# Optimization experiments

Hardware: AMD Instinct MI355X
Metric: run time of the kernel (lower is better)

Reference implementation:

```python
import jax, jax.numpy as jnp
import numpy as np

N = 50000      # nodes
E = 400000     # edges
F = 64         # feature_size
H = 4          # heads
D = 16         # embedding_size (per-head dim)
HD = H * D     # concat hidden = 64
ED = 16        # edge_dim
L = 3          # model_layers (extra TransformerConv layers)
DN = 256       # dense_neurons
G = 128        # number of graphs in the batch
SCALE = float(1.0 / np.sqrt(D))


def setup_inputs() -> dict:
    key = jax.random.key(0)
    ks = jax.random.split(key, 40)

    def w(k, shape, fan_in):
        return jax.random.normal(k, shape, jnp.float32) / np.float32(np.sqrt(fan_in))

    inp = {}
    inp["x"] = jax.random.normal(ks[0], (N, F), jnp.float32)
    inp["edge_attr"] = jax.random.normal(ks[1], (E, ED), jnp.float32)
    inp["edge_index"] = jax.random.randint(ks[2], (2, E), 0, N)
    inp["batch"] = jnp.sort(jax.random.randint(ks[3], (N,), 0, G))

    # conv1: feature_size -> heads*embedding
    inp["Wq0"] = w(ks[4], (F, HD), F); inp["bq0"] = jnp.zeros((HD,), jnp.float32)
    inp["Wk0"] = w(ks[5], (F, HD), F); inp["bk0"] = jnp.zeros((HD,), jnp.float32)
    inp["Wv0"] = w(ks[6], (F, HD), F); inp["bv0"] = jnp.zeros((HD,), jnp.float32)
    inp["We0"] = w(ks[7], (ED, HD), ED)                      # lin_edge, no bias
    inp["Ws0"] = w(ks[8], (F, HD), F); inp["bs0"] = jnp.zeros((HD,), jnp.float32)  # lin_skip
    inp["Wb0"] = w(ks[9], (3 * HD, 1), 3 * HD)               # lin_beta, no bias

    # stacked layers 1..L: heads*embedding -> heads*embedding
    inp["Wq"] = w(ks[10], (L, HD, HD), HD); inp["bq"] = jnp.zeros((L, HD), jnp.float32)
    inp["Wk"] = w(ks[11], (L, HD, HD), HD); inp["bk"] = jnp.zeros((L, HD), jnp.float32)
    inp["Wv"] = w(ks[12], (L, HD, HD), HD); inp["bv"] = jnp.zeros((L, HD), jnp.float32)
    inp["We"] = w(ks[13], (L, ED, HD), ED)
    inp["Ws"] = w(ks[14], (L, HD, HD), HD); inp["bs"] = jnp.zeros((L, HD), jnp.float32)
    inp["Wb"] = w(ks[15], (L, 3 * HD, 1), 3 * HD)

    # MLP head: Linear(2*HD -> DN), Linear(DN -> 1)
    inp["Wlin"] = w(ks[16], (2 * HD, DN), 2 * HD); inp["blin"] = jnp.zeros((DN,), jnp.float32)
    inp["Wout"] = w(ks[17], (DN, 1), DN); inp["bout"] = jnp.zeros((1,), jnp.float32)
    return inp


def _tconv(x, edge_attr, src, dst, Wq, bq, Wk, bk, Wv, bv, We, Ws, bs, Wb):
    """PyG TransformerConv (concat=True, beta=True, edge_dim), eval mode (no dropout)."""
    n = x.shape[0]
    q = (x @ Wq + bq).reshape(n, H, D)
    k = (x @ Wk + bk).reshape(n, H, D)
    v = (x @ Wv + bv).reshape(n, H, D)
    e = (edge_attr @ We).reshape(-1, H, D)
    ke = k[src] + e                                   # [E,H,D] keys with edge feats
    ve = v[src] + e                                   # [E,H,D] values with edge feats
    logits = jnp.einsum('ehd,ehd->eh', q[dst], ke) * SCALE
    # segment softmax over incoming edges of each target node
    m = jax.ops.segment_max(logits, dst, num_segments=n)
    p = jnp.exp(logits - m[dst])
    s = jax.ops.segment_sum(p, dst, num_segments=n)
    a = p / (s[dst] + 1e-16)                          # [E,H]
    agg = jax.ops.segment_sum(a[:, :, None] * ve, dst, num_segments=n).reshape(n, HD)
    skip = x @ Ws + bs                                # root/skip transform
    beta = jax.nn.sigmoid(jnp.concatenate([agg, skip, agg - skip], axis=-1) @ Wb)
    return beta * skip + (1.0 - beta) * agg


def reference(x, edge_attr, edge_index, batch,
              Wq0, bq0, Wk0, bk0, Wv0, bv0, We0, Ws0, bs0, Wb0,
              Wq, bq, Wk, bk, Wv, bv, We, Ws, bs, Wb,
              Wlin, blin, Wout, bout):
    src, dst = edge_index[0], edge_index[1]
    h = jax.nn.relu(_tconv(x, edge_attr, src, dst,
                           Wq0, bq0, Wk0, bk0, Wv0, bv0, We0, Ws0, bs0, Wb0))
    for i in range(L):
        h = jax.nn.relu(_tconv(h, edge_attr, src, dst,
                               Wq[i], bq[i], Wk[i], bk[i], Wv[i], bv[i],
                               We[i], Ws[i], bs[i], Wb[i]))
    # global max pool (gmp) and global mean pool (gap)
    cnt = jax.ops.segment_sum(jnp.ones((h.shape[0],), h.dtype), batch, num_segments=G)
    gmax = jax.ops.segment_max(h, batch, num_segments=G)
    gmax = jnp.where(cnt[:, None] > 0, gmax, 0.0)
    gmean = jax.ops.segment_sum(h, batch, num_segments=G) / jnp.maximum(cnt[:, None], 1.0)
    z = jnp.concatenate([gmax, gmean], axis=-1) @ Wlin + blin
    return jax.nn.sigmoid(z @ Wout + bout)
```

## Files before the change

### kernel.cpp

```cpp
#include <hip/hip_runtime.h>
#include <math.h>

#define SCALEF 0.25f

typedef __attribute__((ext_vector_type(8))) short short8;
typedef __attribute__((ext_vector_type(4))) float f32x4;

__device__ __forceinline__ unsigned short f2bf(float x) {
  unsigned u = __float_as_uint(x);
  unsigned r = u + 0x7FFFu + ((u >> 16) & 1u);
  return (unsigned short)(r >> 16);
}
__device__ __forceinline__ float bf2f(unsigned short h) {
  return __uint_as_float(((unsigned)h) << 16);
}

__global__ void k_hist(const int* __restrict__ dst, int* __restrict__ counts, int E) {
  int i = blockIdx.x * 256 + threadIdx.x;
  if (i < E) atomicAdd(&counts[dst[i]], 1);
}

__global__ __launch_bounds__(1024) void k_scan1(const int* __restrict__ counts,
                                                int* __restrict__ excl,
                                                int* __restrict__ bsums, int n) {
  __shared__ int sd[1024];
  int t = threadIdx.x;
  int i = blockIdx.x * 1024 + t;
  int v = (i < n) ? counts[i] : 0;
  sd[t] = v;
  __syncthreads();
  for (int off = 1; off < 1024; off <<= 1) {
    int x = (t >= off) ? sd[t - off] : 0;
    __syncthreads();
    sd[t] += x;
    __syncthreads();
  }
  if (i < n) excl[i] = sd[t] - v;
  if (t == 1023) bsums[blockIdx.x] = sd[1023];
}

__global__ void k_scan2(int* bsums, int nb) {
  if (threadIdx.x == 0 && blockIdx.x == 0) {
    int run = 0;
    for (int i = 0; i < nb; ++i) { int v = bsums[i]; bsums[i] = run; run += v; }
  }
}

__global__ __launch_bounds__(1024) void k_scan3(int* __restrict__ rowptr, int* __restrict__ cursor,
                                                const int* __restrict__ bsums, int n, int Etot) {
  int i = blockIdx.x * 1024 + threadIdx.x;
  if (i < n) { int v = rowptr[i] + bsums[blockIdx.x]; rowptr[i] = v; cursor[i] = v; }
  if (i == 0) rowptr[n] = Etot;
}

__global__ void k_scatter(const int* __restrict__ dst, int* __restrict__ cursor,
                          int* __restrict__ colidx, int E) {
  int i = blockIdx.x * 256 + threadIdx.x;
  if (i < E) { int pos = atomicAdd(&cursor[dst[i]], 1); colidx[pos] = i; }
}

__global__ void k_perm(const int* __restrict__ colidx, const int* __restrict__ esrc,
                       const float* __restrict__ EA, int* __restrict__ esrcp,
                       unsigned short* __restrict__ EAp, int E) {
  int r = blockIdx.x * 256 + threadIdx.x;
  if (r >= E) return;
  const int eid = colidx[r];
  esrcp[r] = esrc[eid] * 128;
  const float4* s4 = (const float4*)(EA + ((size_t)eid << 4));
  float4 a = s4[0], b = s4[1], c = s4[2], d = s4[3];
  union { unsigned short us[16]; uint4 u4[2]; } o;
  o.us[0] = f2bf(a.x); o.us[1] = f2bf(a.y); o.us[2] = f2bf(a.z); o.us[3] = f2bf(a.w);
  o.us[4] = f2bf(b.x); o.us[5] = f2bf(b.y); o.us[6] = f2bf(b.z); o.us[7] = f2bf(b.w);
  o.us[8] = f2bf(c.x); o.us[9] = f2bf(c.y); o.us[10] = f2bf(c.z); o.us[11] = f2bf(c.w);
  o.us[12] = f2bf(d.x); o.us[13] = f2bf(d.y); o.us[14] = f2bf(d.z); o.us[15] = f2bf(d.w);
  uint4* d4 = (uint4*)(EAp + ((size_t)r << 4));
  d4[0] = o.u4[0]; d4[1] = o.u4[1];
}

__global__ __launch_bounds__(256) void k_wqt(
    const float* __restrict__ Wq0, const float* __restrict__ bq0, const float* __restrict__ We0,
    const float* __restrict__ Wq, const float* __restrict__ bq, const float* __restrict__ We,
    float* __restrict__ Wqt, float* __restrict__ bqt) {
  const int l = blockIdx.x;
  const float* wq = (l == 0) ? Wq0 : Wq + (l - 1) * 4096;
  const float* bv = (l == 0) ? bq0 : bq + (l - 1) * 64;
  const float* we = (l == 0) ? We0 : We + (l - 1) * 1024;
  float* out  = Wqt + l * 4096;
  float* outb = bqt + l * 64;
  const int t = threadIdx.x;
  const int r = t >> 2;
  const int hh = t & 3;
  float wqr[16];
  #pragma unroll
  for (int d = 0; d < 16; ++d) wqr[d] = wq[r * 64 + hh * 16 + d];
  #pragma unroll
  for (int bb = 0; bb < 16; ++bb) {
    float s = 0.f;
    #pragma unroll
    for (int d = 0; d < 16; ++d) s += wqr[d] * we[bb * 64 + hh * 16 + d];
    out[r * 64 + hh * 16 + bb] = s * SCALEF;
  }
  if (r == 0) {
    #pragma unroll
    for (int bb = 0; bb < 16; ++bb) {
      float s = 0.f;
      #pragma unroll
      for (int d = 0; d < 16; ++d) s += bv[hh * 16 + d] * we[bb * 64 + hh * 16 + d];
      outb[hh * 16 + bb] = s * SCALEF;
    }
  }
}

__global__ void k_wprep(
    const float* __restrict__ Wq0, const float* __restrict__ Wk0, const float* __restrict__ Wv0,
    const float* __restrict__ Ws0,
    const float* __restrict__ Wq, const float* __restrict__ Wk, const float* __restrict__ Wv,
    const float* __restrict__ Ws, const float* __restrict__ Wqt,
    const float* __restrict__ bq0, const float* __restrict__ bk0, const float* __restrict__ bv0,
    const float* __restrict__ bs0,
    const float* __restrict__ bq, const float* __restrict__ bk, const float* __restrict__ bv,
    const float* __restrict__ bs, const float* __restrict__ bqt,
    unsigned short* __restrict__ WT, float* __restrict__ bcat) {
  const int id = blockIdx.x * 256 + threadIdx.x;
  if (id >= 4 * 5 * 4096) return;
  const int l = id / 20480;
  const int rem = id - l * 20480;
  const int mat = rem >> 12;
  const int idx = rem & 4095;
  const int k = idx >> 6;
  const int c = idx & 63;
  float v;
  if (mat == 0)      v = (l == 0) ? Wq0[idx] : Wq[(l - 1) * 4096 + idx];
  else if (mat == 1) v = (l == 0) ? Wk0[idx] : Wk[(l - 1) * 4096 + idx];
  else if (mat == 2) v = (l == 0) ? Wv0[idx] : Wv[(l - 1) * 4096 + idx];
  else if (mat == 3) v = (l == 0) ? Ws0[idx] : Ws[(l - 1) * 4096 + idx];
  else               v = Wqt[l * 4096 + idx];
  WT[(size_t)(l * 5 + mat) * 4096 + c * 64 + k] = f2bf(v);
  if (k == 0) {
    float b;
    if (mat == 0)      b = (l == 0) ? bq0[c] : bq[(l - 1) * 64 + c];
    else if (mat == 1) b = (l == 0) ? bk0[c] : bk[(l - 1) * 64 + c];
    else if (mat == 2) b = (l == 0) ? bv0[c] : bv[(l - 1) * 64 + c];
    else if (mat == 3) b = (l == 0) ? bs0[c] : bs[(l - 1) * 64 + c];
    else               b = bqt[l * 64 + c];
    bcat[(l * 5 + mat) * 64 + c] = b;
  }
}

__global__ void k_xcast(const float* __restrict__ x, unsigned short* __restrict__ xb, int n4) {
  int i = blockIdx.x * 256 + threadIdx.x;
  if (i < n4) {
    float4 v = ((const float4*)x)[i];
    ushort4 o;
    o.x = f2bf(v.x); o.y = f2bf(v.y); o.z = f2bf(v.z); o.w = f2bf(v.w);
    ((ushort4*)xb)[i] = o;
  }
}

__global__ __launch_bounds__(256) void k_linm(
    const unsigned short* __restrict__ Xb, const unsigned short* __restrict__ WT,
    const float* __restrict__ bcat,
    unsigned short* __restrict__ Qb, unsigned short* __restrict__ Kb,
    unsigned short* __restrict__ Vb, unsigned short* __restrict__ Sb,
    unsigned short* __restrict__ Tb, int n) {
  const int lane = threadIdx.x & 63;
  const int tile = blockIdx.x * 4 + (threadIdx.x >> 6);
  const int ntr = n >> 4;
  if (tile >= ntr) return;
  const int r0 = tile << 4;
  const int c15 = lane & 15;
  const int kg = lane >> 4;
  const int rbase = r0 + kg * 4;

  const unsigned short* xrow = Xb + (size_t)(r0 + c15) * 64 + kg * 8;
  const short8 a0 = *(const short8*)(xrow);
  const short8 a1 = *(const short8*)(xrow + 32);

  #pragma unroll
  for (int mat = 0; mat < 5; ++mat) {
    const unsigned short* wb = WT + ((size_t)mat << 12) + (size_t)c15 * 64 + kg * 8;
    f32x4 acc0 = {0.f, 0.f, 0.f, 0.f}, acc1 = acc0, acc2 = acc0, acc3 = acc0;
    {
      short8 b0 = *(const short8*)(wb);
      short8 b1 = *(const short8*)(wb + 32);
      acc0 = __builtin_amdgcn_mfma_f32_16x16x32_bf16(a0, b0, acc0, 0, 0, 0);
      acc0 = __builtin_amdgcn_mfma_f32_16x16x32_bf16(a1, b1, acc0, 0, 0, 0);
    }
    {
      short8 b0 = *(const short8*)(wb + 16 * 64);
      short8 b1 = *(const short8*)(wb + 16 * 64 + 32);
      acc1 = __builtin_amdgcn_mfma_f32_16x16x32_bf16(a0, b0, acc1, 0, 0, 0);
      acc1 = __builtin_amdgcn_mfma_f32_16x16x32_bf16(a1, b1, acc1, 0, 0, 0);
    }
    {
      short8 b0 = *(const short8*)(wb + 32 * 64);
      short8 b1 = *(const short8*)(wb + 32 * 64 + 32);
      acc2 = __builtin_amdgcn_mfma_f32_16x16x32_bf16(a0, b0, acc2, 0, 0, 0);
      acc2 = __builtin_amdgcn_mfma_f32_16x16x32_bf16(a1, b1, acc2, 0, 0, 0);
    }
    {
      short8 b0 = *(const short8*)(wb + 48 * 64);
      short8 b1 = *(const short8*)(wb + 48 * 64 + 32);
      acc3 = __builtin_amdgcn_mfma_f32_16x16x32_bf16(a0, b0, acc3, 0, 0, 0);
      acc3 = __builtin_amdgcn_mfma_f32_16x16x32_bf16(a1, b1, acc3, 0, 0, 0);
    }

    const float* bb = bcat + mat * 64;
    const float bi0 = bb[c15], bi1 = bb[16 + c15], bi2 = bb[32 + c15], bi3 = bb[48 + c15];

    unsigned short* O = (mat == 0) ? Qb : (mat == 1) ? Kb : (mat == 2) ? Vb
                      : (mat == 3) ? Sb : Tb;
    #pragma unroll
    for (int reg = 0; reg < 4; ++reg) {
      const size_t ro = (size_t)(rbase + reg) * 64;
      O[ro + c15]      = f2bf(acc0[reg] + bi0);
      O[ro + 16 + c15] = f2bf(acc1[reg] + bi1);
      O[ro + 32 + c15] = f2bf(acc2[reg] + bi2);
      O[ro + 48 + c15] = f2bf(acc3[reg] + bi3);
    }
  }
}

#define LOADST(KK, VV, EE, jj) do {                                       \
    int jc_ = (jj) < mc ? (jj) : mc - 1;                                  \
    int off_ = __builtin_amdgcn_readlane(snv, jc_);                       \
    KK = *(const unsigned short*)(kbase + off_);                          \
    VV = *(const unsigned short*)(vbase + off_);                          \
    EE = eabase[(size_t)(c0 + jc_) << 4];                                 \
  } while (0)

#define COMPUTE(KK, VV, EE, jj) do {                                      \
    if ((jj) < mc) {                                                      \
      const float ef = bf2f(EE);                                          \
      float pl = qv * bf2f(KK) + tl * ef;                                 \
      pl += __shfl_xor(pl, 1, 64);                                        \
      pl += __shfl_xor(pl, 2, 64);                                        \
      pl += __shfl_xor(pl, 4, 64);                                        \
      pl += __shfl_xor(pl, 8, 64);                                        \
      const float p = __expf(pl);                                         \
      ssum += p;                                                          \
      accv += p * bf2f(VV);                                               \
      accw += p * ef;                                                     \
    }                                                                     \
  } while (0)

__global__ __launch_bounds__(128, 6) void k_attn(
    const unsigned short* __restrict__ Qb, const unsigned short* __restrict__ Kb,
    const unsigned short* __restrict__ Vb, const unsigned short* __restrict__ Tb,
    const unsigned short* __restrict__ Sb, const unsigned short* __restrict__ EAp,
    const int* __restrict__ esrcp, const int* __restrict__ rowptr,
    const float* __restrict__ We, const float* __restrict__ Wb,
    unsigned short* __restrict__ Hout, int n) {
  const int t = threadIdx.x;
  const int lane = t & 63;
  const int node = blockIdx.x * 2 + (t >> 6);
  if (node >= n) return;

  const float qv = bf2f(Qb[(size_t)node * 64 + lane]) * SCALEF;
  const float tl = bf2f(Tb[(size_t)node * 64 + lane]);
  const int r0 = rowptr[node], r1 = rowptr[node + 1];

  const char* kbase = (const char*)Kb + 2 * lane;
  const char* vbase = (const char*)Vb + 2 * lane;
  const unsigned short* eabase = EAp + (lane & 15);

  float ssum = 0.f, accv = 0.f, accw = 0.f;

  for (int c0 = r0; c0 < r1; c0 += 64) {
    const int mc = min(64, r1 - c0);
    int snv = 0;
    if (lane < mc) snv = esrcp[c0 + lane];

    unsigned short kA, vA, kB, vB, kC, vC, kD, vD;
    unsigned short eA, eB, eC, eD;
    LOADST(kA, vA, eA, 0);
    LOADST(kB, vB, eB, 1);
    LOADST(kC, vC, eC, 2);
    LOADST(kD, vD, eD, 3);

    for (int j = 0; j < mc; j += 4) {
      COMPUTE(kA, vA, eA, j);     LOADST(kA, vA, eA, j + 4);
      COMPUTE(kB, vB, eB, j + 1); LOADST(kB, vB, eB, j + 5);
      COMPUTE(kC, vC, eC, j + 2); LOADST(kC, vC, eC, j + 6);
      COMPUTE(kD, vD, eD, j + 3); LOADST(kD, vD, eD, j + 7);
    }
  }

  float agg = accv;
  #pragma unroll
  for (int j = 0; j < 16; ++j) {
    const float wj = __shfl(accw, (lane & 48) | j, 64);
    agg += wj * We[j * 64 + lane];
  }
  agg /= (ssum + 1e-16f);

  const float sk = bf2f(Sb[(size_t)node * 64 + lane]);
  float contrib = agg * Wb[lane] + sk * Wb[64 + lane] + (agg - sk) * Wb[128 + lane];
  #pragma unroll
  for (int off = 1; off < 64; off <<= 1) contrib += __shfl_xor(contrib, off, 64);
  const float beta = 1.f / (1.f + __expf(-contrib));
  const float o = beta * sk + (1.f - beta) * agg;
  Hout[(size_t)node * 64 + lane] = f2bf(fmaxf(o, 0.f));
}

__global__ __launch_bounds__(256) void k_pool(const unsigned short* __restrict__ Hf,
    const int* __restrict__ batch,
    float* __restrict__ gmax, float* __restrict__ gmean, int n) {
  const int g = blockIdx.x;
  const int lane = threadIdx.x & 63;
  const int w = threadIdx.x >> 6;

  int a = 0, b = n;
  while (a < b) { int mid = (a + b) >> 1; if (batch[mid] < g) a = mid + 1; else b = mid; }
  const int lo = a;
  b = n;
  while (a < b) { int mid = (a + b) >> 1; if (batch[mid] < g + 1) a = mid + 1; else b = mid; }
  const int hi = a;

  float vmax = -1e30f, vsum = 0.f;
  for (int i = lo + w; i < hi; i += 4) {
    const float v = bf2f(Hf[(size_t)i * 64 + lane]);
    vmax = fmaxf(vmax, v);
    vsum += v;
  }
  __shared__ float smax[4][64], ssum[4][64];
  smax[w][lane] = vmax;
  ssum[w][lane] = vsum;
  __syncthreads();
  if (w == 0) {
    const float mx = fmaxf(fmaxf(smax[0][lane], smax[1][lane]),
                           fmaxf(smax[2][lane], smax[3][lane]));
    const float sm = ssum[0][lane] + ssum[1][lane] + ssum[2][lane] + ssum[3][lane];
    const int cnt = hi - lo;
    gmax[g * 64 + lane]  = (cnt > 0) ? mx : 0.f;
    gmean[g * 64 + lane] = sm / fmaxf((float)cnt, 1.f);
  }
}

__global__ __launch_bounds__(256) void k_mlp(const float* __restrict__ gmax,
    const float* __restrict__ gmean,
    const float* __restrict__ Wlin, const float* __restrict__ blin,
    const float* __restrict__ Wout, const float* __restrict__ bout,
    float* __restrict__ out, int G) {
  __shared__ float cat[128];
  __shared__ float red[4];
  const int g = blockIdx.x;
  const int t = threadIdx.x;
  if (t < 64) cat[t] = gmax[g * 64 + t];
  else if (t < 128) cat[t] = gmean[g * 64 + (t - 64)];
  __syncthreads();
  float acc = blin[t];
  for (int j = 0; j < 128; ++j) acc += cat[j] * Wlin[j * 256 + t];
  float p = acc * Wout[t];
  #pragma unroll
  for (int off = 1; off < 64; off <<= 1) p += __shfl_xor(p, off, 64);
  if ((t & 63) == 0) red[t >> 6] = p;
  __syncthreads();
  if (t == 0) {
    const float z = red[0] + red[1] + red[2] + red[3] + bout[0];
    out[g] = 1.f / (1.f + __expf(-z));
  }
}

extern "C" void kernel_launch(void* const* d_in, const int* in_sizes, int n_in,
                              void* d_out, int out_size, void* d_ws, size_t ws_size,
                              hipStream_t stream) {
  const float* x     = (const float*)d_in[0];
  const float* ea    = (const float*)d_in[1];
  const int*   eidx  = (const int*)d_in[2];
  const int*   batch = (const int*)d_in[3];
  const float *Wq0 = (const float*)d_in[4],  *bq0 = (const float*)d_in[5];
  const float *Wk0 = (const float*)d_in[6],  *bk0 = (const float*)d_in[7];
  const float *Wv0 = (const float*)d_in[8],  *bv0 = (const float*)d_in[9];
  const float *We0 = (const float*)d_in[10];
  const float *Ws0 = (const float*)d_in[11], *bs0 = (const float*)d_in[12];
  const float *Wb0 = (const float*)d_in[13];
  const float *Wq  = (const float*)d_in[14], *bq  = (const float*)d_in[15];
  const float *Wk  = (const float*)d_in[16], *bk  = (const float*)d_in[17];
  const float *Wv  = (const float*)d_in[18], *bv  = (const float*)d_in[19];
  const float *We  = (const float*)d_in[20];
  const float *Ws  = (const float*)d_in[21], *bs  = (const float*)d_in[22];
  const float *Wb  = (const float*)d_in[23];
  const float *Wlin = (const float*)d_in[24], *blin = (const float*)d_in[25];
  const float *Wout = (const float*)d_in[26], *bout = (const float*)d_in[27];

  const int N = in_sizes[0] / 64;
  const int E = in_sizes[2] / 2;
  const int G = out_size;
  const int* esrc = eidx;
  const int* edst = eidx + E;

  char* wsp = (char*)d_ws;
  auto alloc = [&](size_t bytes) -> void* {
    void* p = (void*)wsp;
    wsp += (bytes + 255) & ~(size_t)255;
    return p;
  };
  unsigned short* Qb = (unsigned short*)alloc((size_t)N * 64 * 2);
  unsigned short* Kb = (unsigned short*)alloc((size_t)N * 64 * 2);
  unsigned short* Vb = (unsigned short*)alloc((size_t)N * 64 * 2);
  unsigned short* Tb = (unsigned short*)alloc((size_t)N * 64 * 2);
  unsigned short* Sb16 = (unsigned short*)alloc((size_t)N * 64 * 2);
  unsigned short* Hb16 = (unsigned short*)alloc((size_t)N * 64 * 2);
  unsigned short* Xb16 = (unsigned short*)alloc((size_t)N * 64 * 2);
  int* counts  = (int*)alloc((size_t)N * 4);
  int* rowptr  = (int*)alloc((size_t)(N + 1) * 4);
  int* cursor  = (int*)alloc((size_t)N * 4);
  int* colidx  = (int*)alloc((size_t)E * 4);
  int* bsums   = (int*)alloc(1024 * 4);
  int* esrcp   = (int*)alloc((size_t)E * 4);
  unsigned short* EAp = (unsigned short*)alloc((size_t)E * 16 * 2);
  float* Wqt   = (float*)alloc(4 * 4096 * 4);
  float* bqt   = (float*)alloc(4 * 64 * 4);
  unsigned short* WT = (unsigned short*)alloc(4 * 5 * 4096 * 2);
  float* bcat  = (float*)alloc(4 * 5 * 64 * 4);
  float* gmaxf  = (float*)alloc((size_t)G * 64 * 4);
  float* gmeanf = (float*)alloc((size_t)G * 64 * 4);

  const int gridE = (E + 255) / 256;
  const int NB1 = (N + 1023) / 1024;
  hipMemsetAsync(counts, 0, (size_t)N * 4, stream);
  k_hist<<<gridE, 256, 0, stream>>>(edst, counts, E);
  k_scan1<<<NB1, 1024, 0, stream>>>(counts, rowptr, bsums, N);
  k_scan2<<<1, 64, 0, stream>>>(bsums, NB1);
  k_scan3<<<NB1, 1024, 0, stream>>>(rowptr, cursor, bsums, N, E);
  k_scatter<<<gridE, 256, 0, stream>>>(edst, cursor, colidx, E);
  k_perm<<<gridE, 256, 0, stream>>>(colidx, esrc, ea, esrcp, EAp, E);
  k_wqt<<<4, 256, 0, stream>>>(Wq0, bq0, We0, Wq, bq, We, Wqt, bqt);
  k_wprep<<<(4 * 5 * 4096 + 255) / 256, 256, 0, stream>>>(
      Wq0, Wk0, Wv0, Ws0, Wq, Wk, Wv, Ws, Wqt,
      bq0, bk0, bv0, bs0, bq, bk, bv, bs, bqt, WT, bcat);
  k_xcast<<<(N * 16 + 255) / 256, 256, 0, stream>>>(x, Xb16, N * 16);

  const int gridLinM = ((N >> 4) + 3) / 4;
  const int gridAttn = (N + 1) / 2;
  for (int l = 0; l < 4; ++l) {
    const float* we_ = (l == 0) ? We0 : We + (l - 1) * 1024;
    const float* wb_ = (l == 0) ? Wb0 : Wb + (l - 1) * 192;
    const unsigned short* xin = (l == 0) ? Xb16 : Hb16;
    k_linm<<<gridLinM, 256, 0, stream>>>(xin, WT + (size_t)l * 20480, bcat + l * 320,
                                         Qb, Kb, Vb, Sb16, Tb, N);
    k_attn<<<gridAttn, 128, 0, stream>>>(Qb, Kb, Vb, Tb, Sb16, EAp, esrcp, rowptr,
                                         we_, wb_, Hb16, N);
  }

  k_pool<<<G, 256, 0, stream>>>(Hb16, batch, gmaxf, gmeanf, N);
  k_mlp<<<G, 256, 0, stream>>>(gmaxf, gmeanf, Wlin, blin, Wout, bout,
                               (float*)d_out, G);
}
```

Measured before the change: 408.2 us.

## Interleave K/V storage, fuse scatter/perm, prep/xcast and pool/MLP kernels

K and V projections are now written interleaved per node, so the attention gather fetches both with one 32-bit load per lane instead of two 16-bit loads. The esrcp stride goes from 128 to 256 bytes to match the wider row. The CSR scatter and edge permutation are merged into one kernel, which drops the colidx buffer and one pass over E. The x cast is merged into weight prep, pooling is merged with the MLP, and the single-thread block-sum scan becomes a wavefront shuffle scan. The attention launch-bounds occupancy hint goes from 6 to 8, which may tighten register allocation.

```diff
diff --git a/kernel.cpp b/kernel.cpp
--- a/kernel.cpp
+++ b/kernel.cpp
@@ -39,11 +39,15 @@
   if (t == 1023) bsums[blockIdx.x] = sd[1023];
 }
 
-__global__ void k_scan2(int* bsums, int nb) {
-  if (threadIdx.x == 0 && blockIdx.x == 0) {
-    int run = 0;
-    for (int i = 0; i < nb; ++i) { int v = bsums[i]; bsums[i] = run; run += v; }
-  }
+__global__ __launch_bounds__(64) void k_scan2(int* bsums, int nb) {
+  const int lane = threadIdx.x;
+  int v = (lane < nb) ? bsums[lane] : 0;
+  const int orig = v;
+  for (int off = 1; off < 64; off <<= 1) {
+    int u = __shfl_up(v, off, 64);
+    if (lane >= off) v += u;
+  }
+  if (lane < nb) bsums[lane] = v - orig;
 }
 
 __global__ __launch_bounds__(1024) void k_scan3(int* __restrict__ rowptr, int* __restrict__ cursor,
@@ -53,27 +57,21 @@
   if (i == 0) rowptr[n] = Etot;
 }
 
-__global__ void k_scatter(const int* __restrict__ dst, int* __restrict__ cursor,
-                          int* __restrict__ colidx, int E) {
+__global__ void k_scatperm(const int* __restrict__ esrc, const int* __restrict__ edst,
+                           const float* __restrict__ EA, int* __restrict__ cursor,
+                           int* __restrict__ esrcp, unsigned short* __restrict__ EAp, int E) {
   int i = blockIdx.x * 256 + threadIdx.x;
-  if (i < E) { int pos = atomicAdd(&cursor[dst[i]], 1); colidx[pos] = i; }
-}
-
-__global__ void k_perm(const int* __restrict__ colidx, const int* __restrict__ esrc,
-                       const float* __restrict__ EA, int* __restrict__ esrcp,
-                       unsigned short* __restrict__ EAp, int E) {
-  int r = blockIdx.x * 256 + threadIdx.x;
-  if (r >= E) return;
-  const int eid = colidx[r];
-  esrcp[r] = esrc[eid] * 128;
-  const float4* s4 = (const float4*)(EA + ((size_t)eid << 4));
+  if (i >= E) return;
+  const int pos = atomicAdd(&cursor[edst[i]], 1);
+  esrcp[pos] = esrc[i] * 256;
+  const float4* s4 = (const float4*)(EA + ((size_t)i << 4));
   float4 a = s4[0], b = s4[1], c = s4[2], d = s4[3];
   union { unsigned short us[16]; uint4 u4[2]; } o;
   o.us[0] = f2bf(a.x); o.us[1] = f2bf(a.y); o.us[2] = f2bf(a.z); o.us[3] = f2bf(a.w);
   o.us[4] = f2bf(b.x); o.us[5] = f2bf(b.y); o.us[6] = f2bf(b.z); o.us[7] = f2bf(b.w);
   o.us[8] = f2bf(c.x); o.us[9] = f2bf(c.y); o.us[10] = f2bf(c.z); o.us[11] = f2bf(c.w);
   o.us[12] = f2bf(d.x); o.us[13] = f2bf(d.y); o.us[14] = f2bf(d.z); o.us[15] = f2bf(d.w);
-  uint4* d4 = (uint4*)(EAp + ((size_t)r << 4));
+  uint4* d4 = (uint4*)(EAp + ((size_t)pos << 4));
   d4[0] = o.u4[0]; d4[1] = o.u4[1];
 }
 
@@ -111,7 +109,8 @@
   }
 }
 
-__global__ void k_wprep(
+__global__ void k_prep(
+    const float* __restrict__ x, unsigned short* __restrict__ xb, int n16,
     const float* __restrict__ Wq0, const float* __restrict__ Wk0, const float* __restrict__ Wv0,
     const float* __restrict__ Ws0,
     const float* __restrict__ Wq, const float* __restrict__ Wk, const float* __restrict__ Wv,
@@ -122,47 +121,43 @@
     const float* __restrict__ bs, const float* __restrict__ bqt,
     unsigned short* __restrict__ WT, float* __restrict__ bcat) {
   const int id = blockIdx.x * 256 + threadIdx.x;
-  if (id >= 4 * 5 * 4096) return;
-  const int l = id / 20480;
-  const int rem = id - l * 20480;
-  const int mat = rem >> 12;
-  const int idx = rem & 4095;
-  const int k = idx >> 6;
-  const int c = idx & 63;
-  float v;
-  if (mat == 0)      v = (l == 0) ? Wq0[idx] : Wq[(l - 1) * 4096 + idx];
-  else if (mat == 1) v = (l == 0) ? Wk0[idx] : Wk[(l - 1) * 4096 + idx];
-  else if (mat == 2) v = (l == 0) ? Wv0[idx] : Wv[(l - 1) * 4096 + idx];
-  else if (mat == 3) v = (l == 0) ? Ws0[idx] : Ws[(l - 1) * 4096 + idx];
-  else               v = Wqt[l * 4096 + idx];
-  WT[(size_t)(l * 5 + mat) * 4096 + c * 64 + k] = f2bf(v);
-  if (k == 0) {
-    float b;
-    if (mat == 0)      b = (l == 0) ? bq0[c] : bq[(l - 1) * 64 + c];
-    else if (mat == 1) b = (l == 0) ? bk0[c] : bk[(l - 1) * 64 + c];
-    else if (mat == 2) b = (l == 0) ? bv0[c] : bv[(l - 1) * 64 + c];
-    else if (mat == 3) b = (l == 0) ? bs0[c] : bs[(l - 1) * 64 + c];
-    else               b = bqt[l * 64 + c];
-    bcat[(l * 5 + mat) * 64 + c] = b;
-  }
-}
-
-__global__ void k_xcast(const float* __restrict__ x, unsigned short* __restrict__ xb, int n4) {
-  int i = blockIdx.x * 256 + threadIdx.x;
-  if (i < n4) {
-    float4 v = ((const float4*)x)[i];
+  if (id < n16) {
+    float4 v = ((const float4*)x)[id];
     ushort4 o;
     o.x = f2bf(v.x); o.y = f2bf(v.y); o.z = f2bf(v.z); o.w = f2bf(v.w);
-    ((ushort4*)xb)[i] = o;
+    ((ushort4*)xb)[id] = o;
+  }
+  if (id < 4 * 5 * 4096) {
+    const int l = id / 20480;
+    const int rem = id - l * 20480;
+    const int mat = rem >> 12;
+    const int idx = rem & 4095;
+    const int k = idx >> 6;
+    const int c = idx & 63;
+    float v;
+    if (mat == 0)      v = (l == 0) ? Wq0[idx] : Wq[(l - 1) * 4096 + idx];
+    else if (mat == 1) v = (l == 0) ? Wk0[idx] : Wk[(l - 1) * 4096 + idx];
+    else if (mat == 2) v = (l == 0) ? Wv0[idx] : Wv[(l - 1) * 4096 + idx];
+    else if (mat == 3) v = (l == 0) ? Ws0[idx] : Ws[(l - 1) * 4096 + idx];
+    else               v = Wqt[l * 4096 + idx];
+    WT[(size_t)(l * 5 + mat) * 4096 + c * 64 + k] = f2bf(v);
+    if (k == 0) {
+      float b;
+      if (mat == 0)      b = (l == 0) ? bq0[c] : bq[(l - 1) * 64 + c];
+      else if (mat == 1) b = (l == 0) ? bk0[c] : bk[(l - 1) * 64 + c];
+      else if (mat == 2) b = (l == 0) ? bv0[c] : bv[(l - 1) * 64 + c];
+      else if (mat == 3) b = (l == 0) ? bs0[c] : bs[(l - 1) * 64 + c];
+      else               b = bqt[l * 64 + c];
+      bcat[(l * 5 + mat) * 64 + c] = b;
+    }
   }
 }
 
 __global__ __launch_bounds__(256) void k_linm(
     const unsigned short* __restrict__ Xb, const unsigned short* __restrict__ WT,
     const float* __restrict__ bcat,
-    unsigned short* __restrict__ Qb, unsigned short* __restrict__ Kb,
-    unsigned short* __restrict__ Vb, unsigned short* __restrict__ Sb,
-    unsigned short* __restrict__ Tb, int n) {
+    unsigned short* __restrict__ Qb, unsigned short* __restrict__ KV16,
+    unsigned short* __restrict__ Sb, unsigned short* __restrict__ Tb, int n) {
   const int lane = threadIdx.x & 63;
   const int tile = blockIdx.x * 4 + (threadIdx.x >> 6);
   const int ntr = n >> 4;
@@ -208,46 +203,58 @@
     const float* bb = bcat + mat * 64;
     const float bi0 = bb[c15], bi1 = bb[16 + c15], bi2 = bb[32 + c15], bi3 = bb[48 + c15];
 
-    unsigned short* O = (mat == 0) ? Qb : (mat == 1) ? Kb : (mat == 2) ? Vb
-                      : (mat == 3) ? Sb : Tb;
-    #pragma unroll
-    for (int reg = 0; reg < 4; ++reg) {
-      const size_t ro = (size_t)(rbase + reg) * 64;
-      O[ro + c15]      = f2bf(acc0[reg] + bi0);
-      O[ro + 16 + c15] = f2bf(acc1[reg] + bi1);
-      O[ro + 32 + c15] = f2bf(acc2[reg] + bi2);
-      O[ro + 48 + c15] = f2bf(acc3[reg] + bi3);
-    }
-  }
-}
-
-#define LOADST(KK, VV, EE, jj) do {                                       \
+    if (mat == 1 || mat == 2) {
+      unsigned short* O = KV16 + (mat == 2 ? 1 : 0);
+      #pragma unroll
+      for (int reg = 0; reg < 4; ++reg) {
+        const size_t ro = (size_t)(rbase + reg) * 128;
+        O[ro + 2 * c15]        = f2bf(acc0[reg] + bi0);
+        O[ro + 2 * (16 + c15)] = f2bf(acc1[reg] + bi1);
+        O[ro + 2 * (32 + c15)] = f2bf(acc2[reg] + bi2);
+        O[ro + 2 * (48 + c15)] = f2bf(acc3[reg] + bi3);
+      }
+    } else {
+      unsigned short* O = (mat == 0) ? Qb : (mat == 3) ? Sb : Tb;
+      #pragma unroll
+      for (int reg = 0; reg < 4; ++reg) {
+        const size_t ro = (size_t)(rbase + reg) * 64;
+        O[ro + c15]      = f2bf(acc0[reg] + bi0);
+        O[ro + 16 + c15] = f2bf(acc1[reg] + bi1);
+        O[ro + 32 + c15] = f2bf(acc2[reg] + bi2);
+        O[ro + 48 + c15] = f2bf(acc3[reg] + bi3);
+      }
+    }
+  }
+}
+
+#define LOADST(KV, EE, jj) do {                                           \
     int jc_ = (jj) < mc ? (jj) : mc - 1;                                  \
     int off_ = __builtin_amdgcn_readlane(snv, jc_);                       \
-    KK = *(const unsigned short*)(kbase + off_);                          \
-    VV = *(const unsigned short*)(vbase + off_);                          \
+    KV = *(const unsigned int*)(kvbase + off_);                           \
     EE = eabase[(size_t)(c0 + jc_) << 4];                                 \
   } while (0)
 
-#define COMPUTE(KK, VV, EE, jj) do {                                      \
+#define COMPUTE(KV, EE, jj) do {                                          \
     if ((jj) < mc) {                                                      \
       const float ef = bf2f(EE);                                          \
-      float pl = qv * bf2f(KK) + tl * ef;                                 \
+      const float kf = __uint_as_float(KV << 16);                         \
+      const float vf = __uint_as_float(KV & 0xFFFF0000u);                 \
+      float pl = qv * kf + tl * ef;                                       \
       pl += __shfl_xor(pl, 1, 64);                                        \
       pl += __shfl_xor(pl, 2, 64);                                        \
       pl += __shfl_xor(pl, 4, 64);                                        \
       pl += __shfl_xor(pl, 8, 64);                                        \
       const float p = __expf(pl);                                         \
       ssum += p;                                                          \
-      accv += p * bf2f(VV);                                               \
+      accv += p * vf;                                                     \
       accw += p * ef;                                                     \
     }                                                                     \
   } while (0)
 
-__global__ __launch_bounds__(128, 6) void k_attn(
-    const unsigned short* __restrict__ Qb, const unsigned short* __restrict__ Kb,
-    const unsigned short* __restrict__ Vb, const unsigned short* __restrict__ Tb,
-    const unsigned short* __restrict__ Sb, const unsigned short* __restrict__ EAp,
+__global__ __launch_bounds__(128, 8) void k_attn(
+    const unsigned short* __restrict__ Qb, const unsigned short* __restrict__ KV16,
+    const unsigned short* __restrict__ Tb, const unsigned short* __restrict__ Sb,
+    const unsigned short* __restrict__ EAp,
     const int* __restrict__ esrcp, const int* __restrict__ rowptr,
     const float* __restrict__ We, const float* __restrict__ Wb,
     unsigned short* __restrict__ Hout, int n) {
@@ -260,8 +267,7 @@
   const float tl = bf2f(Tb[(size_t)node * 64 + lane]);
   const int r0 = rowptr[node], r1 = rowptr[node + 1];
 
-  const char* kbase = (const char*)Kb + 2 * lane;
-  const char* vbase = (const char*)Vb + 2 * lane;
+  const char* kvbase = (const char*)KV16 + 4 * lane;
   const unsigned short* eabase = EAp + (lane & 15);
 
   float ssum = 0.f, accv = 0.f, accw = 0.f;
@@ -271,18 +277,18 @@
     int snv = 0;
     if (lane < mc) snv = esrcp[c0 + lane];
 
-    unsigned short kA, vA, kB, vB, kC, vC, kD, vD;
+    unsigned int kvA, kvB, kvC, kvD;
     unsigned short eA, eB, eC, eD;
-    LOADST(kA, vA, eA, 0);
-    LOADST(kB, vB, eB, 1);
-    LOADST(kC, vC, eC, 2);
-    LOADST(kD, vD, eD, 3);
+    LOADST(kvA, eA, 0);
+    LOADST(kvB, eB, 1);
+    LOADST(kvC, eC, 2);
+    LOADST(kvD, eD, 3);
 
     for (int j = 0; j < mc; j += 4) {
-      COMPUTE(kA, vA, eA, j);     LOADST(kA, vA, eA, j + 4);
-      COMPUTE(kB, vB, eB, j + 1); LOADST(kB, vB, eB, j + 5);
-      COMPUTE(kC, vC, eC, j + 2); LOADST(kC, vC, eC, j + 6);
-      COMPUTE(kD, vD, eD, j + 3); LOADST(kD, vD, eD, j + 7);
+      COMPUTE(kvA, eA, j);     LOADST(kvA, eA, j + 4);
+      COMPUTE(kvB, eB, j + 1); LOADST(kvB, eB, j + 5);
+      COMPUTE(kvC, eC, j + 2); LOADST(kvC, eC, j + 6);
+      COMPUTE(kvD, eD, j + 3); LOADST(kvD, eD, j + 7);
     }
   }
 
@@ -303,12 +309,15 @@
   Hout[(size_t)node * 64 + lane] = f2bf(fmaxf(o, 0.f));
 }
 
-__global__ __launch_bounds__(256) void k_pool(const unsigned short* __restrict__ Hf,
+__global__ __launch_bounds__(256) void k_poolmlp(const unsigned short* __restrict__ Hf,
     const int* __restrict__ batch,
-    float* __restrict__ gmax, float* __restrict__ gmean, int n) {
+    const float* __restrict__ Wlin, const float* __restrict__ blin,
+    const float* __restrict__ Wout, const float* __restrict__ bout,
+    float* __restrict__ out, int n) {
   const int g = blockIdx.x;
-  const int lane = threadIdx.x & 63;
-  const int w = threadIdx.x >> 6;
+  const int t = threadIdx.x;
+  const int lane = t & 63;
+  const int w = t >> 6;
 
   int a = 0, b = n;
   while (a < b) { int mid = (a + b) >> 1; if (batch[mid] < g) a = mid + 1; else b = mid; }
@@ -324,6 +333,7 @@
     vsum += v;
   }
   __shared__ float smax[4][64], ssum[4][64];
+  __shared__ float cat[128];
   smax[w][lane] = vmax;
   ssum[w][lane] = vsum;
   __syncthreads();
@@ -332,28 +342,17 @@
                            fmaxf(smax[2][lane], smax[3][lane]));
     const float sm = ssum[0][lane] + ssum[1][lane] + ssum[2][lane] + ssum[3][lane];
     const int cnt = hi - lo;
-    gmax[g * 64 + lane]  = (cnt > 0) ? mx : 0.f;
-    gmean[g * 64 + lane] = sm / fmaxf((float)cnt, 1.f);
-  }
-}
-
-__global__ __launch_bounds__(256) void k_mlp(const float* __restrict__ gmax,
-    const float* __restrict__ gmean,
-    const float* __restrict__ Wlin, const float* __restrict__ blin,
-    const float* __restrict__ Wout, const float* __restrict__ bout,
-    float* __restrict__ out, int G) {
-  __shared__ float cat[128];
-  __shared__ float red[4];
-  const int g = blockIdx.x;
-  const int t = threadIdx.x;
-  if (t < 64) cat[t] = gmax[g * 64 + t];
-  else if (t < 128) cat[t] = gmean[g * 64 + (t - 64)];
+    cat[lane]      = (cnt > 0) ? mx : 0.f;
+    cat[64 + lane] = sm / fmaxf((float)cnt, 1.f);
+  }
   __syncthreads();
+
   float acc = blin[t];
   for (int j = 0; j < 128; ++j) acc += cat[j] * Wlin[j * 256 + t];
   float p = acc * Wout[t];
   #pragma unroll
   for (int off = 1; off < 64; off <<= 1) p += __shfl_xor(p, off, 64);
+  __shared__ float red[4];
   if ((t & 63) == 0) red[t >> 6] = p;
   __syncthreads();
   if (t == 0) {
@@ -397,8 +396,7 @@
     return p;
   };
   unsigned short* Qb = (unsigned short*)alloc((size_t)N * 64 * 2);
-  unsigned short* Kb = (unsigned short*)alloc((size_t)N * 64 * 2);
-  unsigned short* Vb = (unsigned short*)alloc((size_t)N * 64 * 2);
+  unsigned short* KV16 = (unsigned short*)alloc((size_t)N * 64 * 4);
   unsigned short* Tb = (unsigned short*)alloc((size_t)N * 64 * 2);
   unsigned short* Sb16 = (unsigned short*)alloc((size_t)N * 64 * 2);
   unsigned short* Hb16 = (unsigned short*)alloc((size_t)N * 64 * 2);
@@ -406,7 +404,6 @@
   int* counts  = (int*)alloc((size_t)N * 4);
   int* rowptr  = (int*)alloc((size_t)(N + 1) * 4);
   int* cursor  = (int*)alloc((size_t)N * 4);
-  int* colidx  = (int*)alloc((size_t)E * 4);
   int* bsums   = (int*)alloc(1024 * 4);
   int* esrcp   = (int*)alloc((size_t)E * 4);
   unsigned short* EAp = (unsigned short*)alloc((size_t)E * 16 * 2);
@@ -414,8 +411,6 @@
   float* bqt   = (float*)alloc(4 * 64 * 4);
   unsigned short* WT = (unsigned short*)alloc(4 * 5 * 4096 * 2);
   float* bcat  = (float*)alloc(4 * 5 * 64 * 4);
-  float* gmaxf  = (float*)alloc((size_t)G * 64 * 4);
-  float* gmeanf = (float*)alloc((size_t)G * 64 * 4);
 
   const int gridE = (E + 255) / 256;
   const int NB1 = (N + 1023) / 1024;
@@ -424,13 +419,12 @@
   k_scan1<<<NB1, 1024, 0, stream>>>(counts, rowptr, bsums, N);
   k_scan2<<<1, 64, 0, stream>>>(bsums, NB1);
   k_scan3<<<NB1, 1024, 0, stream>>>(rowptr, cursor, bsums, N, E);
-  k_scatter<<<gridE, 256, 0, stream>>>(edst, cursor, colidx, E);
-  k_perm<<<gridE, 256, 0, stream>>>(colidx, esrc, ea, esrcp, EAp, E);
+  k_scatperm<<<gridE, 256, 0, stream>>>(esrc, edst, ea, cursor, esrcp, EAp, E);
   k_wqt<<<4, 256, 0, stream>>>(Wq0, bq0, We0, Wq, bq, We, Wqt, bqt);
-  k_wprep<<<(4 * 5 * 4096 + 255) / 256, 256, 0, stream>>>(
+  k_prep<<<(N * 16 + 255) / 256, 256, 0, stream>>>(
+      x, Xb16, N * 16,
       Wq0, Wk0, Wv0, Ws0, Wq, Wk, Wv, Ws, Wqt,
       bq0, bk0, bv0, bs0, bq, bk, bv, bs, bqt, WT, bcat);
-  k_xcast<<<(N * 16 + 255) / 256, 256, 0, stream>>>(x, Xb16, N * 16);
 
   const int gridLinM = ((N >> 4) + 3) / 4;
   const int gridAttn = (N + 1) / 2;
@@ -439,12 +433,11 @@
     const float* wb_ = (l == 0) ? Wb0 : Wb + (l - 1) * 192;
     const unsigned short* xin = (l == 0) ? Xb16 : Hb16;
     k_linm<<<gridLinM, 256, 0, stream>>>(xin, WT + (size_t)l * 20480, bcat + l * 320,
-                                         Qb, Kb, Vb, Sb16, Tb, N);
-    k_attn<<<gridAttn, 128, 0, stream>>>(Qb, Kb, Vb, Tb, Sb16, EAp, esrcp, rowptr,
+                                         Qb, KV16, Sb16, Tb, N);
+    k_attn<<<gridAttn, 128, 0, stream>>>(Qb, KV16, Tb, Sb16, EAp, esrcp, rowptr,
                                          we_, wb_, Hb16, N);
   }
 
-  k_pool<<<G, 256, 0, stream>>>(Hb16, batch, gmaxf, gmeanf, N);
-  k_mlp<<<G, 256, 0, stream>>>(gmaxf, gmeanf, Wlin, blin, Wout, bout,
-                               (float*)d_out, G);
-}
+  k_poolmlp<<<G, 256, 0, stream>>>(Hb16, batch, Wlin, blin, Wout, bout,
+                                   (float*)d_out, N);
+}
```

Result: faster. 371.5 us (-9.0%).
